# Performance work log

Hardware: AMD Instinct MI355X
Metric: run time of the kernel (lower is better)

The kernel has to match this reference:

```python
import jax, jax.numpy as jnp
import numpy as np

# module hyperparameters (match init_kwargs)
IN_PLANES = 64
OUT = 64            # out_planes
N_HASHES = 4
CHUNK = 25          # chunk_size
GROUPS = 8
KS = 56             # kernel_size == attended axis length H
GP = OUT // GROUPS  # group_planes = 8
EPS_N = 5e-5        # F.normalize eps
BN_EPS = 1e-5
F_GW, F_GV1, F_GV2 = 0.1, 0.1, 1.0


def l2norm(x, axis):
    # torch F.normalize(p=2, eps=EPS_N)
    n = jnp.sqrt(jnp.sum(x * x, axis=axis, keepdims=True))
    return x / jnp.maximum(n, EPS_N)


def setup_inputs() -> dict:
    key = jax.random.key(0)
    k1, k2, k3, k4 = jax.random.split(key, 4)
    x = jax.random.normal(k1, (2, IN_PLANES, KS, 56), jnp.float32)
    conv_w = jax.random.normal(k2, (OUT * 3 // 2, IN_PLANES), jnp.float32) * np.float32(np.sqrt(1.0 / IN_PLANES))
    bn_gamma = jnp.ones((OUT * 3 // 2,), jnp.float32)
    bn_beta = jnp.zeros((OUT * 3 // 2,), jnp.float32)
    relative = jax.random.normal(k3, (KS, GP * 3 // 2), jnp.float32) * np.float32(np.sqrt(1.0 / GP))
    # LSH random rotations: hash_buckets = min(56//25 + (56//25)%2, 10) = 2 -> hb//2 = 1
    rotations = jax.random.normal(k4, (OUT // 2, N_HASHES, 1), jnp.float32)
    return dict(x=x, conv_w=conv_w, bn_gamma=bn_gamma, bn_beta=bn_beta,
                relative=relative, rotations=rotations)


def reference(x, conv_w, bn_gamma, bn_beta, relative, rotations):
    # width=False: (N,C,H,W) -> (N,W,C,H), flatten batch with W
    N, C, Hax, W = x.shape
    x = jnp.transpose(x, (0, 3, 1, 2)).reshape(N * W, C, Hax)
    B, H = N * W, Hax
    hash_buckets = min(H // CHUNK + (H // CHUNK) % 2, 10)

    # 1x1 conv + eval-mode BatchNorm (running_mean=0, running_var=1)
    qkv = jnp.einsum('oc,bch->boh', conv_w, x)
    qkv = qkv / np.float32(np.sqrt(1.0 + BN_EPS)) * bn_gamma[None, :, None] + bn_beta[None, :, None]
    # NOTE: original uses raw reshape (B,C3,H) -> (B,H,C3), NOT a transpose
    qkv = qkv.reshape(B, H, OUT * 3 // 2)
    w_match = qkv[..., :OUT // 2]   # (B,H,out/2)
    v_match = qkv[..., OUT // 2:]   # (B,H,out)
    w_emb = relative[:, :GP // 2]
    v_emb = relative[:, GP // 2:]

    # LSH hashing (rotations shared across batch)
    rot = jnp.einsum('btf,fhi->bhti', w_match, rotations)
    rot = jnp.concatenate([rot, -rot], axis=-1)           # (B,nh,H,hash_buckets)
    codes = jnp.argmax(rot, axis=-1)
    codes = codes + (jnp.arange(N_HASHES) * hash_buckets)[None, :, None]
    codes = codes.reshape(B, N_HASHES * H)

    indices = jnp.argsort(codes, axis=-1)                 # stable sort into buckets
    undo = jnp.argsort(indices, axis=-1)
    mod = indices % H
    w_s = jnp.take_along_axis(w_match, mod[:, :, None], axis=1)
    v_s = jnp.take_along_axis(v_match, mod[:, :, None], axis=1)

    padding = (CHUNK - H % CHUNK) % CHUNK                 # 19 here
    w_b = w_s.reshape(B, N_HASHES, H, OUT // 2)
    v_b = v_s.reshape(B, N_HASHES, H, OUT)
    if padding:
        w_b = jnp.concatenate([w_b, w_b[:, :, -padding:, :]], axis=2)
        v_b = jnp.concatenate([v_b, v_b[:, :, -padding:, :]], axis=2)
        w_emb = jnp.concatenate([w_emb, w_emb[-padding:, :]], axis=0)
        v_emb = jnp.concatenate([v_emb, v_emb[-padding:, :]], axis=0)
    # raw reshapes, exactly as torch does (groups folded via flat reshape)
    w_b = w_b.reshape(B, GROUPS, N_HASHES, -1, CHUNK, GP // 2)
    v_b = v_b.reshape(B, GROUPS, N_HASHES, -1, CHUNK, GP)
    w_emb = w_emb.reshape(-1, CHUNK, GP // 2)             # (K,25,4)
    v_emb = v_emb.reshape(-1, CHUNK, GP)                  # (K,25,8)
    K = w_emb.shape[0]

    def adj(t):  # look-around over the chunk axis (dim 3), cat on dim 4
        return jnp.concatenate([t, jnp.roll(t, 1, axis=3), jnp.roll(t, -1, axis=3)], axis=4)

    def adj_emb(t):
        return jnp.concatenate([t, jnp.roll(t, 1, axis=0), jnp.roll(t, -1, axis=0)], axis=1)

    w_m = adj(l2norm(w_b, -1))
    v_a = adj(v_b)
    w_e = adj_emb(w_emb)
    v_e = adj_emb(v_emb)

    raw = jnp.einsum('bghkie,bghkje->bghkij', w_b, w_m)            # (B,g,h,K,25,75)
    emb_sc = F_GW * jnp.einsum('bghkie,kje->bghkij', w_b, w_e)
    ss = jnp.concatenate([raw, emb_sc], axis=1)                    # (B,2g,h,K,25,75)
    ss = l2norm(ss, 1).reshape(B, 2, GROUPS, N_HASHES, K, CHUNK, CHUNK * 3).sum(axis=1)

    bs = jax.nn.logsumexp(ss, axis=-1, keepdims=True)
    score = jnp.exp(ss - bs)
    bs = bs.reshape(B, GROUPS, N_HASHES, K * CHUNK)

    r_out = F_GV2 * jnp.einsum('bgukij,bgukje->bgukie', score, v_a)
    r_emb = F_GV1 * jnp.einsum('bgukij,kje->bgukie', score, v_e)
    ret = jnp.concatenate([r_out, r_emb], axis=-1)                 # (B,g,h,K,25,2*gp)
    ret = ret.reshape(B, N_HASHES, K, CHUNK, OUT * 2)              # raw reshape
    ret = ret.reshape(B, OUT * 2, N_HASHES, K, CHUNK)              # raw reshape
    ret = l2norm(ret, 1).reshape(B, N_HASHES, K, CHUNK, OUT, 2).sum(axis=-1)
    bs = l2norm(bs, 1).sum(axis=1)                                 # (B,h,K*25)

    ret = ret.reshape(B, N_HASHES, K * CHUNK, OUT)
    if padding:
        ret = ret[:, :, :-padding, :]
        bs = bs[:, :, :-padding]
    ret = ret.reshape(B, N_HASHES * H, OUT)
    bs = bs.reshape(B, N_HASHES * H)

    ret = jnp.take_along_axis(ret, undo[:, :, None], axis=1)      # unsort
    bs = jnp.take_along_axis(bs, undo, axis=1)
    ret = ret.reshape(B, N_HASHES, H, OUT)
    bs = bs.reshape(B, N_HASHES, H, 1)

    probs = jax.nn.softmax(bs, axis=1)
    ret = jnp.sum(ret * probs, axis=1)                             # (B,H,out)
    ret = ret.reshape(N, W, H, OUT)
    return jnp.transpose(ret, (0, 3, 2, 1))                        # (N,out,H,W)
```

## Files before the change

### kernel.cpp

```cpp
#include <hip/hip_runtime.h>
#include <math.h>


#define EPSN 5e-5f
#define INV_EPSN 20000.0f
#define LOG2E 1.4426950408889634f
#define LN2   0.6931471805599453f

__device__ __forceinline__ float dot4(const float4 a, const float4 b) {
    return a.x * b.x + a.y * b.y + a.z * b.z + a.w * b.w;
}
__device__ __forceinline__ void fma4(float4& a, float s, const float4 v) {
    a.x += s * v.x; a.y += s * v.y; a.z += s * v.z; a.w += s * v.w;
}

__global__ __launch_bounds__(256) void k12_qkv_sort(
        const float* __restrict__ x, const float* __restrict__ cw,
        const float* __restrict__ gamma, const float* __restrict__ beta,
        const float* __restrict__ rot, float* __restrict__ qkv,
        int* __restrict__ idx_buf) {
    __shared__ float xsT[56 * 68];
    __shared__ float cws[96 * 64];
    __shared__ float wm[56 * 32];
    __shared__ float rl[128];
    __shared__ float gs[96], bt[96];
    __shared__ int code[224];
    __shared__ int srt[224];
    const int b = blockIdx.x, n = b / 56, w = b % 56, tid = threadIdx.x;
    const float* xb = x + n * 200704 + w;
    #pragma unroll 7
    for (int i = tid; i < 3584; i += 256) {
        int c = i / 56, h = i % 56;
        xsT[h * 68 + c] = xb[c * 3136 + h * 56];
    }
    #pragma unroll 8
    for (int i = tid; i < 6144; i += 256) cws[i] = cw[i];
    if (tid < 128) rl[tid] = rot[tid];
    if (tid < 96) { gs[tid] = gamma[tid]; bt[tid] = beta[tid]; }
    __syncthreads();
    const float inv_s = 1.0f / sqrtf(1.0f + 1.0e-5f);
    for (int tl = tid; tl < 1344; tl += 256) {
        int oq = tl / 56, h = tl % 56;
        int o0 = oq * 4;
        float s0 = 0.f, s1 = 0.f, s2 = 0.f, s3 = 0.f;
        #pragma unroll
        for (int cs = 0; cs < 16; ++cs) {
            float4 xv = *(const float4*)&xsT[h * 68 + cs * 4];
            float4 c0 = *(const float4*)&cws[(o0 + 0) * 64 + cs * 4];
            float4 c1 = *(const float4*)&cws[(o0 + 1) * 64 + cs * 4];
            float4 c2 = *(const float4*)&cws[(o0 + 2) * 64 + cs * 4];
            float4 c3 = *(const float4*)&cws[(o0 + 3) * 64 + cs * 4];
            s0 += dot4(xv, c0); s1 += dot4(xv, c1);
            s2 += dot4(xv, c2); s3 += dot4(xv, c3);
        }
        #pragma unroll
        for (int qq = 0; qq < 4; ++qq) {
            int o = o0 + qq;
            float sv = (qq == 0) ? s0 : (qq == 1) ? s1 : (qq == 2) ? s2 : s3;
            float val = sv * inv_s * gs[o] + bt[o];
            int j = o * 56 + h;
            qkv[b * 5376 + j] = val;
            int f = j % 96;
            if (f < 32) wm[(j / 96) * 32 + f] = val;
        }
    }
    __syncthreads();
    if (tid < 224) {
        int u = tid / 56, t = tid % 56;
        float s = 0.f;
        #pragma unroll 8
        for (int f = 0; f < 32; ++f) s += wm[t * 32 + f] * rl[f * 4 + u];
        code[tid] = ((s < 0.f) ? 1 : 0) + 2 * u;
    }
    __syncthreads();
    if (tid < 224) {
        int c = code[tid], r = 0;
        #pragma unroll 8
        for (int p = 0; p < 224; ++p) {
            int cp = code[p];
            r += (int)((cp < c) | ((cp == c) & (p < tid)));
        }
        srt[r] = tid;
    }
    __syncthreads();
    if (tid < 224) idx_buf[b * 224 + tid] = srt[tid];
}

__global__ __launch_bounds__(256) void k3_attn(
        const float* __restrict__ qkv, const int* __restrict__ idx_buf,
        const float* __restrict__ rel, float* __restrict__ Rb,
        float* __restrict__ bsb) {
    __shared__ __align__(16) float Wc[8][3][25][4];
    __shared__ __align__(16) float Vb[8][3][25][8];
    __shared__ __align__(16) float WbK[8][25][4];
    __shared__ float DIT[75][25];
    __shared__ int ibL[224];
    const int b = blockIdx.x, u = blockIdx.y, k = blockIdx.z;
    const int tid = threadIdx.x;
    const float* q = qkv + b * 5376;

    if (tid < 224) ibL[tid] = idx_buf[b * 224 + tid];
    __syncthreads();

    #pragma unroll 3
    for (int idx = tid; idx < 600; idx += 256) {
        int i = idx % 25, kk = (idx / 25) % 3, g = idx / 75;
        int p0 = 1200 * g + 300 * u + 100 * kk + 4 * i;
        int h = p0 / 2400, r = p0 % 2400, t = r >> 5, f = r & 31;
        int row = (t < 56) ? t : t - 19;
        int tt = ibL[h * 56 + row] % 56;
        float4 v = *(const float4*)&q[tt * 96 + f];
        if (kk == k) *(float4*)&WbK[g][i][0] = v;
        float ni = fminf(__builtin_amdgcn_rsqf(dot4(v, v)), INV_EPSN);
        v.x *= ni; v.y *= ni; v.z *= ni; v.w *= ni;
        *(float4*)&Wc[g][kk][i][0] = v;
    }
    #pragma unroll 5
    for (int idx = tid; idx < 1200; idx += 256) {
        int half = idx & 1, fr = idx >> 1;
        int i = fr % 25, kk = (fr / 25) % 3, g = fr / 75;
        int p0 = 2400 * g + 600 * u + 200 * kk + 8 * i + 4 * half;
        int h = p0 / 4800, r = p0 % 4800, t = r >> 6, f = r & 63;
        int row = (t < 56) ? t : t - 19;
        int tt = ibL[h * 56 + row] % 56;
        *(float4*)&Vb[g][kk][i][4 * half] = *(const float4*)&q[tt * 96 + 32 + f];
    }
    __syncthreads();

    if (tid < 250) {
        const int i = tid % 25, jg = tid / 25;
        float4 wb8[8];
        #pragma unroll
        for (int g = 0; g < 8; ++g) wb8[g] = *(const float4*)&WbK[g][i][0];
        #pragma unroll
        for (int it = 0; it < 8; ++it) {
            int j = jg * 8 + it;
            if (j < 75) {
                int ks = j / 25, jj = j % 25;
                int roww = (j < 56) ? j : j - 19;
                float4 we = *(const float4*)&rel[roww * 12];
                we.x *= 0.1f; we.y *= 0.1f; we.z *= 0.1f; we.w *= 0.1f;
                float s2 = 0.f;
                #pragma unroll
                for (int g = 0; g < 8; ++g) {
                    float4 wcn = *(const float4*)&Wc[g][ks][jj][0];
                    float raw = dot4(wb8[g], wcn);
                    float emb = dot4(wb8[g], we);
                    s2 += raw * raw + emb * emb;
                }
                DIT[j][i] = fminf(__builtin_amdgcn_rsqf(s2), INV_EPSN);
            }
        }
    }
    __syncthreads();

    #pragma unroll 3
    for (int idx = tid; idx < 600; idx += 256) {
        int i = idx % 25, kk = (idx / 25) % 3, g = idx / 75;
        int tw = kk * 25 + i;
        int roww = (tw < 56) ? tw : tw - 19;
        float4 we = *(const float4*)&rel[roww * 12];
        float4 v = *(const float4*)&Wc[g][kk][i][0];
        v.x += 0.1f * we.x; v.y += 0.1f * we.y;
        v.z += 0.1f * we.z; v.w += 0.1f * we.w;
        *(float4*)&Wc[g][kk][i][0] = v;
    }
    __syncthreads();

    if (tid < 200) {
        const int g = tid & 7, i = tid >> 3;
        const float4 wbr = *(const float4*)&WbK[g][i][0];
        float se = 0.f;
        float4 a0 = {0,0,0,0}, a1 = {0,0,0,0}, a2 = {0,0,0,0}, a3 = {0,0,0,0};
        #pragma unroll
        for (int ks = 0; ks < 3; ++ks) {
            #pragma unroll
            for (int jj = 0; jj < 25; ++jj) {
                const int jP = ks * 25 + jj;
                const int roww = (jP < 56) ? jP : jP - 19;
                float di = DIT[jP][i];
                float e = __builtin_amdgcn_exp2f(
                    dot4(wbr, *(const float4*)&Wc[g][ks][jj][0]) * di * LOG2E);
                se += e;
                const float4* vv = (const float4*)&Vb[g][ks][jj][0];
                fma4(a0, e, vv[0]); fma4(a1, e, vv[1]);
                float4 ve0 = *(const float4*)&rel[roww * 12 + 4];
                float4 ve1 = *(const float4*)&rel[roww * 12 + 8];
                fma4(a2, e, ve0); fma4(a3, e, ve1);
            }
        }
        bsb[b * 2400 + g * 300 + u * 75 + k * 25 + i] =
            __builtin_amdgcn_logf(se) * LN2;
        const float rinv = 1.0f / se;
        const float r2 = 0.1f * rinv;
        a0.x *= rinv; a0.y *= rinv; a0.z *= rinv; a0.w *= rinv;
        a1.x *= rinv; a1.y *= rinv; a1.z *= rinv; a1.w *= rinv;
        a2.x *= r2;   a2.y *= r2;   a2.z *= r2;   a2.w *= r2;
        a3.x *= r2;   a3.y *= r2;   a3.z *= r2;   a3.w *= r2;
        float* rp = Rb + b * 38400 + 4800 * g + 1200 * u + 400 * k + 16 * i;
        ((float4*)rp)[0] = a0;
        ((float4*)rp)[1] = a1;
        ((float4*)rp)[2] = a2;
        ((float4*)rp)[3] = a3;
    }
}

__global__ __launch_bounds__(256) void k45_post(
        const float* __restrict__ Rb, const float* __restrict__ bsb,
        const int* __restrict__ idx_buf, float* __restrict__ out) {
    __shared__ float D[300];
    __shared__ float bsn[300];
    __shared__ float retU[224][32];
    __shared__ float bsU[224];
    __shared__ int idxL[224];
    const int b = blockIdx.x, oh = blockIdx.y, tid = threadIdx.x;
    const int n = b / 56, w = b % 56, o0 = oh * 32;
    const float* R = Rb + b * 38400;
    if (tid < 224) idxL[tid] = idx_buf[b * 224 + tid];
    for (int r = tid; r < 300; r += 256) {
        float s = 0.f;
        #pragma unroll 16
        for (int c = 0; c < 128; ++c) { float v = R[c * 300 + r]; s += v * v; }
        D[r] = fminf(__builtin_amdgcn_rsqf(s), INV_EPSN);
    }
    for (int idx = tid; idx < 300; idx += 256) {
        int u = idx / 75, t = idx % 75;
        float s2 = 0.f, sum = 0.f;
        #pragma unroll
        for (int g = 0; g < 8; ++g) {
            float v = bsb[b * 2400 + g * 300 + u * 75 + t];
            s2 += v * v; sum += v;
        }
        bsn[idx] = sum / fmaxf(sqrtf(s2), EPSN);
    }
    __syncthreads();
    if (tid < 224) {
        int u3 = tid / 56, t = tid % 56;
        bsU[idxL[tid]] = bsn[u3 * 75 + t];
    }
    #pragma unroll 4
    for (int idx = tid; idx < 224 * 32; idx += 256) {
        int p = idx >> 5, oc = idx & 31;
        int o = o0 + oc;
        int u3 = p / 56, t = p % 56;
        int k3 = t / 25, i3 = t % 25;
        int q0 = 9600 * u3 + 3200 * k3 + 128 * i3 + 2 * o;
        float2 rv = *(const float2*)&R[q0];
        int r0 = q0 % 300;
        float val = rv.x * D[r0] + rv.y * D[r0 + 1];
        retU[idxL[p]][oc] = val;
    }
    __syncthreads();
    for (int idx = tid; idx < 56 * 32; idx += 256) {
        int h = idx >> 5, oc = idx & 31;
        int o = o0 + oc;
        float b0 = bsU[h], b1 = bsU[56 + h], b2 = bsU[112 + h], b3 = bsU[168 + h];
        float m = fmaxf(fmaxf(b0, b1), fmaxf(b2, b3));
        float e0 = __builtin_amdgcn_exp2f((b0 - m) * LOG2E);
        float e1 = __builtin_amdgcn_exp2f((b1 - m) * LOG2E);
        float e2 = __builtin_amdgcn_exp2f((b2 - m) * LOG2E);
        float e3 = __builtin_amdgcn_exp2f((b3 - m) * LOG2E);
        float ps = e0 + e1 + e2 + e3;
        float val = (retU[h][oc] * e0 + retU[56 + h][oc] * e1 +
                     retU[112 + h][oc] * e2 + retU[168 + h][oc] * e3) / ps;
        out[((n * 64 + o) * 56 + h) * 56 + w] = val;
    }
}

extern "C" void kernel_launch(void* const* d_in, const int* in_sizes, int n_in,
                              void* d_out, int out_size, void* d_ws, size_t ws_size,
                              hipStream_t stream) {
    (void)in_sizes; (void)n_in; (void)out_size; (void)ws_size;
    const float* x     = (const float*)d_in[0];
    const float* cw    = (const float*)d_in[1];
    const float* gamma = (const float*)d_in[2];
    const float* beta  = (const float*)d_in[3];
    const float* rel   = (const float*)d_in[4];
    const float* rot   = (const float*)d_in[5];
    float* ws  = (float*)d_ws;
    float* qkv = ws;
    float* bsb = ws + 602112;
    float* Rb  = ws + 870912;
    int*   idx = (int*)(ws + 5171712);

    k12_qkv_sort<<<112, 256, 0, stream>>>(x, cw, gamma, beta, rot, qkv, idx);
    k3_attn<<<dim3(112, 4, 3), 256, 0, stream>>>(qkv, idx, rel, Rb, bsb);
    k45_post<<<dim3(112, 2), 256, 0, stream>>>(Rb, bsb, idx, (float*)d_out);
}
```

Baseline: 154.5 us.

## Pre-transpose input, fold embedding into Wc, and reduce bucket scores in attention

After: 322.3 us. +108.6%, slower.

```diff
diff --git a/kernel.cpp b/kernel.cpp
--- a/kernel.cpp
+++ b/kernel.cpp
@@ -14,8 +14,27 @@
     a.x += s * v.x; a.y += s * v.y; a.z += s * v.z; a.w += s * v.w;
 }
 
+__global__ __launch_bounds__(256) void k0_xT(
+        const float* __restrict__ x, float* __restrict__ xT) {
+    __shared__ float T[64][57];
+    const int n = blockIdx.x, h = blockIdx.y, tid = threadIdx.x;
+    const float* xb = x + n * 200704 + h * 56;
+    #pragma unroll 7
+    for (int i = tid; i < 3584; i += 256) {
+        int c = i / 56, w = i % 56;
+        T[c][w] = xb[c * 3136 + w];
+    }
+    __syncthreads();
+    float* xo = xT + n * 200704 + h * 3584;
+    #pragma unroll 7
+    for (int i = tid; i < 3584; i += 256) {
+        int w = i / 64, c = i % 64;
+        xo[w * 64 + c] = T[c][w];
+    }
+}
+
 __global__ __launch_bounds__(256) void k12_qkv_sort(
-        const float* __restrict__ x, const float* __restrict__ cw,
+        const float* __restrict__ xT, const float* __restrict__ cw,
         const float* __restrict__ gamma, const float* __restrict__ beta,
         const float* __restrict__ rot, float* __restrict__ qkv,
         int* __restrict__ idx_buf) {
@@ -27,11 +46,12 @@
     __shared__ int code[224];
     __shared__ int srt[224];
     const int b = blockIdx.x, n = b / 56, w = b % 56, tid = threadIdx.x;
-    const float* xb = x + n * 200704 + w;
-    #pragma unroll 7
-    for (int i = tid; i < 3584; i += 256) {
-        int c = i / 56, h = i % 56;
-        xsT[h * 68 + c] = xb[c * 3136 + h * 56];
+    const float* xTb = xT + n * 200704 + w * 64;
+    #pragma unroll 4
+    for (int i = tid; i < 896; i += 256) {
+        int h = i / 16, cq = i % 16;
+        *(float4*)&xsT[h * 68 + cq * 4] =
+            *(const float4*)&xTb[h * 3584 + cq * 4];
     }
     #pragma unroll 8
     for (int i = tid; i < 6144; i += 256) cws[i] = cw[i];
@@ -89,12 +109,12 @@
 __global__ __launch_bounds__(256) void k3_attn(
         const float* __restrict__ qkv, const int* __restrict__ idx_buf,
         const float* __restrict__ rel, float* __restrict__ Rb,
-        float* __restrict__ bsb) {
-    __shared__ __align__(16) float Wc[8][3][25][4];
+        float* __restrict__ bsnW) {
+    __shared__ __align__(16) float WcF[8][3][25][4];
     __shared__ __align__(16) float Vb[8][3][25][8];
-    __shared__ __align__(16) float WbK[8][25][4];
-    __shared__ float DIT[75][25];
-    __shared__ int ibL[224];
+    __shared__ float nrm[8][25];
+    __shared__ __align__(16) float DIT[75][25];
+    int* ibL = (int*)&DIT[0][0];
     const int b = blockIdx.x, u = blockIdx.y, k = blockIdx.z;
     const int tid = threadIdx.x;
     const float* q = qkv + b * 5376;
@@ -110,10 +130,15 @@
         int row = (t < 56) ? t : t - 19;
         int tt = ibL[h * 56 + row] % 56;
         float4 v = *(const float4*)&q[tt * 96 + f];
-        if (kk == k) *(float4*)&WbK[g][i][0] = v;
-        float ni = fminf(__builtin_amdgcn_rsqf(dot4(v, v)), INV_EPSN);
-        v.x *= ni; v.y *= ni; v.z *= ni; v.w *= ni;
-        *(float4*)&Wc[g][kk][i][0] = v;
+        float len = fmaxf(sqrtf(dot4(v, v)), EPSN);
+        float ni = 1.0f / len;
+        int tw = kk * 25 + i, roww = (tw < 56) ? tw : tw - 19;
+        float4 we = *(const float4*)&rel[roww * 12];
+        float4 o;
+        o.x = v.x * ni + 0.1f * we.x; o.y = v.y * ni + 0.1f * we.y;
+        o.z = v.z * ni + 0.1f * we.z; o.w = v.w * ni + 0.1f * we.w;
+        *(float4*)&WcF[g][kk][i][0] = o;
+        if (kk == k) nrm[g][i] = len;
     }
     #pragma unroll 5
     for (int idx = tid; idx < 1200; idx += 256) {
@@ -129,23 +154,32 @@
 
     if (tid < 250) {
         const int i = tid % 25, jg = tid / 25;
+        const int twi = k * 25 + i;
+        const int rowwi = (twi < 56) ? twi : twi - 19;
+        const float4 wei = *(const float4*)&rel[rowwi * 12];
         float4 wb8[8];
         #pragma unroll
-        for (int g = 0; g < 8; ++g) wb8[g] = *(const float4*)&WbK[g][i][0];
+        for (int g = 0; g < 8; ++g) {
+            float4 t = *(const float4*)&WcF[g][k][i][0];
+            float nr = nrm[g][i];
+            wb8[g].x = (t.x - 0.1f * wei.x) * nr;
+            wb8[g].y = (t.y - 0.1f * wei.y) * nr;
+            wb8[g].z = (t.z - 0.1f * wei.z) * nr;
+            wb8[g].w = (t.w - 0.1f * wei.w) * nr;
+        }
         #pragma unroll
         for (int it = 0; it < 8; ++it) {
             int j = jg * 8 + it;
             if (j < 75) {
                 int ks = j / 25, jj = j % 25;
                 int roww = (j < 56) ? j : j - 19;
-                float4 we = *(const float4*)&rel[roww * 12];
-                we.x *= 0.1f; we.y *= 0.1f; we.z *= 0.1f; we.w *= 0.1f;
+                float4 wej = *(const float4*)&rel[roww * 12];
                 float s2 = 0.f;
                 #pragma unroll
                 for (int g = 0; g < 8; ++g) {
-                    float4 wcn = *(const float4*)&Wc[g][ks][jj][0];
-                    float raw = dot4(wb8[g], wcn);
-                    float emb = dot4(wb8[g], we);
+                    float dF = dot4(wb8[g], *(const float4*)&WcF[g][ks][jj][0]);
+                    float emb = 0.1f * dot4(wb8[g], wej);
+                    float raw = dF - emb;
                     s2 += raw * raw + emb * emb;
                 }
                 DIT[j][i] = fminf(__builtin_amdgcn_rsqf(s2), INV_EPSN);
@@ -154,22 +188,20 @@
     }
     __syncthreads();
 
-    #pragma unroll 3
-    for (int idx = tid; idx < 600; idx += 256) {
-        int i = idx % 25, kk = (idx / 25) % 3, g = idx / 75;
-        int tw = kk * 25 + i;
-        int roww = (tw < 56) ? tw : tw - 19;
-        float4 we = *(const float4*)&rel[roww * 12];
-        float4 v = *(const float4*)&Wc[g][kk][i][0];
-        v.x += 0.1f * we.x; v.y += 0.1f * we.y;
-        v.z += 0.1f * we.z; v.w += 0.1f * we.w;
-        *(float4*)&Wc[g][kk][i][0] = v;
-    }
-    __syncthreads();
-
     if (tid < 200) {
         const int g = tid & 7, i = tid >> 3;
-        const float4 wbr = *(const float4*)&WbK[g][i][0];
+        const int twi = k * 25 + i;
+        const int rowwi = (twi < 56) ? twi : twi - 19;
+        const float4 wei = *(const float4*)&rel[rowwi * 12];
+        float4 wbr;
+        {
+            float4 t = *(const float4*)&WcF[g][k][i][0];
+            float nr = nrm[g][i];
+            wbr.x = (t.x - 0.1f * wei.x) * nr;
+            wbr.y = (t.y - 0.1f * wei.y) * nr;
+            wbr.z = (t.z - 0.1f * wei.z) * nr;
+            wbr.w = (t.w - 0.1f * wei.w) * nr;
+        }
         float se = 0.f;
         float4 a0 = {0,0,0,0}, a1 = {0,0,0,0}, a2 = {0,0,0,0}, a3 = {0,0,0,0};
         #pragma unroll
@@ -178,9 +210,9 @@
             for (int jj = 0; jj < 25; ++jj) {
                 const int jP = ks * 25 + jj;
                 const int roww = (jP < 56) ? jP : jP - 19;
-                float di = DIT[jP][i];
                 float e = __builtin_amdgcn_exp2f(
-                    dot4(wbr, *(const float4*)&Wc[g][ks][jj][0]) * di * LOG2E);
+                    dot4(wbr, *(const float4*)&WcF[g][ks][jj][0])
+                    * DIT[jP][i] * LOG2E);
                 se += e;
                 const float4* vv = (const float4*)&Vb[g][ks][jj][0];
                 fma4(a0, e, vv[0]); fma4(a1, e, vv[1]);
@@ -189,8 +221,13 @@
                 fma4(a2, e, ve0); fma4(a3, e, ve1);
             }
         }
-        bsb[b * 2400 + g * 300 + u * 75 + k * 25 + i] =
-            __builtin_amdgcn_logf(se) * LN2;
+        float bs = __builtin_amdgcn_logf(se) * LN2;
+        float s1 = bs, s2 = bs * bs;
+        s1 += __shfl_xor(s1, 1); s2 += __shfl_xor(s2, 1);
+        s1 += __shfl_xor(s1, 2); s2 += __shfl_xor(s2, 2);
+        s1 += __shfl_xor(s1, 4); s2 += __shfl_xor(s2, 4);
+        if (g == 0)
+            bsnW[b * 300 + u * 75 + k * 25 + i] = s1 / fmaxf(sqrtf(s2), EPSN);
         const float rinv = 1.0f / se;
         const float r2 = 0.1f * rinv;
         a0.x *= rinv; a0.y *= rinv; a0.z *= rinv; a0.w *= rinv;
@@ -205,11 +242,10 @@
     }
 }
 
-__global__ __launch_bounds__(256) void k45_post(
-        const float* __restrict__ Rb, const float* __restrict__ bsb,
+__global__ __launch_bounds__(512) void k45_post(
+        const float* __restrict__ Rb, const float* __restrict__ bsnW,
         const int* __restrict__ idx_buf, float* __restrict__ out) {
     __shared__ float D[300];
-    __shared__ float bsn[300];
     __shared__ float retU[224][32];
     __shared__ float bsU[224];
     __shared__ int idxL[224];
@@ -217,29 +253,19 @@
     const int n = b / 56, w = b % 56, o0 = oh * 32;
     const float* R = Rb + b * 38400;
     if (tid < 224) idxL[tid] = idx_buf[b * 224 + tid];
-    for (int r = tid; r < 300; r += 256) {
+    if (tid < 300) {
         float s = 0.f;
         #pragma unroll 16
-        for (int c = 0; c < 128; ++c) { float v = R[c * 300 + r]; s += v * v; }
-        D[r] = fminf(__builtin_amdgcn_rsqf(s), INV_EPSN);
-    }
-    for (int idx = tid; idx < 300; idx += 256) {
-        int u = idx / 75, t = idx % 75;
-        float s2 = 0.f, sum = 0.f;
-        #pragma unroll
-        for (int g = 0; g < 8; ++g) {
-            float v = bsb[b * 2400 + g * 300 + u * 75 + t];
-            s2 += v * v; sum += v;
-        }
-        bsn[idx] = sum / fmaxf(sqrtf(s2), EPSN);
+        for (int c = 0; c < 128; ++c) { float v = R[c * 300 + tid]; s += v * v; }
+        D[tid] = fminf(__builtin_amdgcn_rsqf(s), INV_EPSN);
     }
     __syncthreads();
     if (tid < 224) {
         int u3 = tid / 56, t = tid % 56;
-        bsU[idxL[tid]] = bsn[u3 * 75 + t];
+        bsU[idxL[tid]] = bsnW[b * 300 + u3 * 75 + t];
     }
     #pragma unroll 4
-    for (int idx = tid; idx < 224 * 32; idx += 256) {
+    for (int idx = tid; idx < 224 * 32; idx += 512) {
         int p = idx >> 5, oc = idx & 31;
         int o = o0 + oc;
         int u3 = p / 56, t = p % 56;
@@ -251,7 +277,7 @@
         retU[idxL[p]][oc] = val;
     }
     __syncthreads();
-    for (int idx = tid; idx < 56 * 32; idx += 256) {
+    for (int idx = tid; idx < 56 * 32; idx += 512) {
         int h = idx >> 5, oc = idx & 31;
         int o = o0 + oc;
         float b0 = bsU[h], b1 = bsU[56 + h], b2 = bsU[112 + h], b3 = bsU[168 + h];
@@ -279,11 +305,13 @@
     const float* rot   = (const float*)d_in[5];
     float* ws  = (float*)d_ws;
     float* qkv = ws;
-    float* bsb = ws + 602112;
+    float* bsn = ws + 602112;
     float* Rb  = ws + 870912;
+    float* xT  = Rb;
     int*   idx = (int*)(ws + 5171712);
 
-    k12_qkv_sort<<<112, 256, 0, stream>>>(x, cw, gamma, beta, rot, qkv, idx);
-    k3_attn<<<dim3(112, 4, 3), 256, 0, stream>>>(qkv, idx, rel, Rb, bsb);
-    k45_post<<<dim3(112, 2), 256, 0, stream>>>(Rb, bsb, idx, (float*)d_out);
-}
+    k0_xT<<<dim3(2, 56), 256, 0, stream>>>(x, xT);
+    k12_qkv_sort<<<112, 256, 0, stream>>>(xT, cw, gamma, beta, rot, qkv, idx);
+    k3_attn<<<dim3(112, 4, 3), 256, 0, stream>>>(qkv, idx, rel, Rb, bsn);
+    k45_post<<<dim3(112, 2), 512, 0, stream>>>(Rb, bsn, idx, (float*)d_out);
+}
```
